# Optimization experiments

Hardware: AMD Instinct MI355X
Metric: run time of the kernel (lower is better)

## Reference

```python
import jax, jax.numpy as jnp
import numpy as np
from jax import lax

DEPTH = 3  # signature truncation depth
B, L, I, H, O = 256, 512, 32, 16, 10
SIG_DIM = H + H**2 + H**3  # 4368 = signatory.signature_channels(16, 3)


def setup_inputs() -> dict:
    key = jax.random.key(0)
    ks = jax.random.split(key, 7)
    s = 1.0 / np.sqrt(H).astype(np.float32)
    sf = 1.0 / np.sqrt(SIG_DIM).astype(np.float32)
    return {
        "X": jax.random.normal(ks[0], (B, L, I), jnp.float32),
        "W_ih": jax.random.uniform(ks[1], (4 * H, I), jnp.float32, -s, s),
        "W_hh": jax.random.uniform(ks[2], (4 * H, H), jnp.float32, -s, s),
        "b_ih": jax.random.uniform(ks[3], (4 * H,), jnp.float32, -s, s),
        "b_hh": jax.random.uniform(ks[4], (4 * H,), jnp.float32, -s, s),
        "fc_w": jax.random.uniform(ks[5], (O, SIG_DIM), jnp.float32, -sf, sf),
        "fc_b": jax.random.uniform(ks[6], (O,), jnp.float32, -sf, sf),
    }


def _lstm(X, W_ih, W_hh, b_ih, b_hh):
    # torch nn.LSTM, single layer, batch_first, gate order (i, f, g, o)
    b, l, _ = X.shape
    h0 = jnp.zeros((b, H), X.dtype)
    c0 = jnp.zeros((b, H), X.dtype)
    # precompute input projection for all timesteps: [L, B, 4H]
    xw = jnp.swapaxes(jnp.einsum('bli,gi->blg', X, W_ih) + b_ih + b_hh, 0, 1)

    def step(carry, xw_t):
        h, c = carry
        gates = xw_t + h @ W_hh.T
        i, f, g, o = jnp.split(gates, 4, axis=-1)
        c = jax.nn.sigmoid(f) * c + jax.nn.sigmoid(i) * jnp.tanh(g)
        h = jax.nn.sigmoid(o) * jnp.tanh(c)
        return (h, c), h

    _, hs = lax.scan(step, (h0, c0), xw)  # hs: [L, B, H]
    return jnp.swapaxes(hs, 0, 1)  # [B, L, H]


def _outer(a, b):
    # batched flattened tensor product: [B, m] x [B, n] -> [B, m*n]
    return (a[:, :, None] * b[:, None, :]).reshape(a.shape[0], -1)


def _signature(h, depth):
    # signatory.signature: Chen's identity scan over path increments,
    # returns concatenated levels 1..depth: [B, C + C^2 + ... + C^depth]
    b, l, c = h.shape
    dx = jnp.swapaxes(h[:, 1:] - h[:, :-1], 0, 1)  # [L-1, B, C]
    S0 = tuple(jnp.zeros((b, c ** (k + 1)), h.dtype) for k in range(depth))

    def step(S, d):
        # exp(d) levels: e_k = d^{tensor k} / k!
        e = [d]
        for k in range(2, depth + 1):
            e.append(_outer(e[-1], d) / k)
        # S <- S (x) exp(d), truncated:  newS_k = S_k + sum_{j=1..k-1} S_{k-j} (x) e_j + e_k
        newS = []
        for k in range(1, depth + 1):
            acc = S[k - 1] + e[k - 1]
            for j in range(1, k):
                acc = acc + _outer(S[k - j - 1], e[j - 1])
            newS.append(acc)
        return tuple(newS), None

    S, _ = lax.scan(step, S0, dx)
    return jnp.concatenate(S, axis=-1)  # [B, SIG_DIM]


def reference(X, W_ih, W_hh, b_ih, b_hh, fc_w, fc_b):
    hseq = _lstm(X, W_ih, W_hh, b_ih, b_hh)           # [B, L, H]
    sig = _signature(hseq, DEPTH)                      # [B, SIG_DIM]
    out = sig @ fc_w.T + fc_b                          # [B, O]
    return out.reshape(-1, O)
```

## Files before the change

### kernel.cpp

```cpp
#include <hip/hip_runtime.h>

#define NB 256
#define NL 512
#define NI 32
#define NH 16
#define NG 64
#define SIGD 4368

__device__ __forceinline__ float RL(float v, int lane) {
  return __builtin_bit_cast(float, __builtin_amdgcn_readlane(__builtin_bit_cast(int, v), lane));
}
template<int CTRL>
__device__ __forceinline__ float QB(float v) {
  return __builtin_bit_cast(float, __builtin_amdgcn_update_dpp(
      0, __builtin_bit_cast(int, v), CTRL, 0xF, 0xF, true));
}
__device__ __forceinline__ int cutf(int k) {
  switch (k) {
    case 1: return 71;  case 2: return 142; case 3: return 212; case 4: return 282;
    case 5: return 352; case 6: return 422; case 7: return 493; case 8: return 511;
    default: return 0;
  }
}

__global__ __launch_bounds__(512, 1) void k_main(const float* __restrict__ X,
    const float* __restrict__ Wih, const float* __restrict__ bih,
    const float* __restrict__ bhh, const float* __restrict__ Whh,
    const float* __restrict__ fcw, const float* __restrict__ fcb,
    float* __restrict__ out) {
  __shared__ __align__(16) float xwh[NL * NG];
  __shared__ __align__(16) float bnd[144];
  __shared__ int prog;
  int tid = threadIdx.x;
  int wv = tid >> 6;
  int ln = tid & 63;
  int b = blockIdx.x;

  if (tid == 0) prog = -1;

  {
    float w2[NI];
#pragma unroll
    for (int i = 0; i < 8; ++i) {
      float4 v = *(const float4*)(Wih + ln * NI + 4 * i);
      w2[4*i+0] = v.x; w2[4*i+1] = v.y; w2[4*i+2] = v.z; w2[4*i+3] = v.w;
    }
    float bias = bih[ln] + bhh[ln];
    const float* xb = X + (size_t)b * NL * NI;
#pragma unroll 4
    for (int t = 64 * wv; t < 64 * (wv + 1); ++t) {
      const float4* xr = (const float4*)(xb + t * NI);
      float x0 = bias, x1 = 0.f, x2 = 0.f, x3 = 0.f;
#pragma unroll
      for (int i = 0; i < 8; ++i) {
        float4 xv = xr[i];
        x0 += xv.x * w2[4*i+0]; x1 += xv.y * w2[4*i+1];
        x2 += xv.z * w2[4*i+2]; x3 += xv.w * w2[4*i+3];
      }
      xwh[t * NG + ln] = (x0 + x1) + (x2 + x3);
    }
  }
  __syncthreads();

  if (wv == 0) {
    const int q = ln & 3;
    const int j = ln >> 2;
    const int gmem = q * 16 + j;
    float w[NH];
#pragma unroll
    for (int qq = 0; qq < 4; ++qq) {
      float4 v = *(const float4*)(Whh + gmem * NH + 4 * qq);
      w[4*qq+0] = v.x; w[4*qq+1] = v.y; w[4*qq+2] = v.z; w[4*qq+3] = v.w;
    }
    const bool isg = (q == 2);
    const float K  = isg ? 2.885390082f : -1.442695041f;
    const float Av = isg ? -2.0f : 1.0f;
    const float Bv = isg ? 1.0f : 0.0f;
    float c = 0.0f, hval = 0.0f;
    float xpre[4];
#pragma unroll
    for (int k = 0; k < 4; ++k) xpre[k] = xwh[k * NG + gmem];
    for (int tb = 0; tb < NL; tb += 16) {
#pragma unroll
      for (int k = 0; k < 16; ++k) {
        int t = tb + k;
        float xval = xpre[k & 3];
        float a0 = xval, a1 = 0.f, a2 = 0.f, a3 = 0.f;
#pragma unroll
        for (int jj = 0; jj < 4; ++jj) {
          a0 += RL(hval, 16*jj + 0)  * w[4*jj + 0];
          a1 += RL(hval, 16*jj + 4)  * w[4*jj + 1];
          a2 += RL(hval, 16*jj + 8)  * w[4*jj + 2];
          a3 += RL(hval, 16*jj + 12) * w[4*jj + 3];
        }
        if (t + 4 < NL) xpre[k & 3] = xwh[(t + 4) * NG + gmem];
        float acc = (a0 + a1) + (a2 + a3);
        float e = __builtin_amdgcn_exp2f(K * acc);
        float r = __builtin_amdgcn_rcpf(1.0f + e);
        float val = __builtin_fmaf(Av, r, Bv);
        float iv = QB<0x00>(val);
        float fv = QB<0x55>(val);
        float gv = QB<0xAA>(val);
        float ov = QB<0xFF>(val);
        c = __builtin_fmaf(fv, c, iv * gv);
        float e2 = __builtin_amdgcn_exp2f(2.885390082f * c);
        float tc = __builtin_fmaf(-2.0f, __builtin_amdgcn_rcpf(1.0f + e2), 1.0f);
        hval = ov * tc;
        if (q == 0) xwh[t * NG + j] = hval;
      }
      __asm__ __volatile__("" ::: "memory");
      if (ln == 0) *(volatile int*)&prog = tb + 15;
    }
  }

  const int bi = ln & 15;
  const int hi = ln >> 4;
  const int ch = (wv == 0) ? 7 : (wv - 1);
  int ts = cutf(ch);
  int te = cutf(ch + 1);
  while (*(volatile int*)&prog < ts) __builtin_amdgcn_s_sleep(1);
  __asm__ __volatile__("" ::: "memory");

  float s3[4][16];
  float s2[4] = {0.f, 0.f, 0.f, 0.f};
#pragma unroll
  for (int m = 0; m < 4; ++m)
#pragma unroll
    for (int cc = 0; cc < 16; ++cc) s3[m][cc] = 0.f;
  float hc[16];
#pragma unroll
  for (int qq = 0; qq < 4; ++qq) {
    float4 v = *(const float4*)(xwh + ts * NG + 4 * qq);
    hc[4*qq+0]=v.x; hc[4*qq+1]=v.y; hc[4*qq+2]=v.z; hc[4*qq+3]=v.w;
  }
  float hcb = xwh[ts * NG + bi];
  float hca[4], h0a[4];
#pragma unroll
  for (int m = 0; m < 4; ++m) { hca[m] = xwh[ts * NG + 4 * m + hi]; h0a[m] = hca[m]; }
  for (int t = ts; t < te; ++t) {
    while (*(volatile int*)&prog < t + 1) __builtin_amdgcn_s_sleep(1);
    __asm__ __volatile__("" ::: "memory");
    const float* rn = xwh + (t + 1) * NG;
    float hn[16];
#pragma unroll
    for (int qq = 0; qq < 4; ++qq) {
      float4 v = *(const float4*)(rn + 4 * qq);
      hn[4*qq+0]=v.x; hn[4*qq+1]=v.y; hn[4*qq+2]=v.z; hn[4*qq+3]=v.w;
    }
    float hnb = rn[bi];
    float d[16];
#pragma unroll
    for (int cc = 0; cc < 16; ++cc) d[cc] = hn[cc] - hc[cc];
    float db = hnb - hcb;
    float P[4];
#pragma unroll
    for (int m = 0; m < 4; ++m) {
      float hna = rn[4 * m + hi];
      float da = hna - hca[m];
      float s1 = hca[m] - h0a[m];
      P[m] = s2[m] + db * (0.5f * s1 + 0.166666666667f * da);
      s2[m] += db * (s1 + 0.5f * da);
      hca[m] = hna;
    }
#pragma unroll
    for (int m = 0; m < 4; ++m)
#pragma unroll
      for (int cc = 0; cc < 16; ++cc)
        s3[m][cc] += P[m] * d[cc];
#pragma unroll
    for (int cc = 0; cc < 16; ++cc) hc[cc] = hn[cc];
    hcb = hnb;
  }
  __syncthreads();

  if (tid < 144) {
    int k = tid >> 4, j = tid & 15;
    bnd[tid] = xwh[cutf(k) * NG + j];
  }
  __syncthreads();

  float* slot0 = xwh;
  float* slot1 = xwh + 4352;
  float* sigb  = xwh + 8704;
  auto writeSlot = [&](float* slot) {
#pragma unroll
    for (int m = 0; m < 4; ++m) slot[64 * m + ln] = s2[m];
    float* s3s = slot + 256;
#pragma unroll
    for (int m = 0; m < 4; ++m)
#pragma unroll
      for (int cc = 0; cc < 16; ++cc)
        s3s[64 * ln + ((m * 16 + cc) ^ (ln & 31))] = s3[m][cc];
  };
  auto combineSlot = [&](const float* slot, int as_, int ae_, int bs_, int be_) {
    const float* s2b = slot;
    const float* s3b = slot + 256;
    float s1b[16];
#pragma unroll
    for (int cc = 0; cc < 16; ++cc) s1b[cc] = bnd[be_ * 16 + cc] - bnd[bs_ * 16 + cc];
    float s1bb = bnd[be_ * 16 + bi] - bnd[bs_ * 16 + bi];
    float s1aa[4];
#pragma unroll
    for (int m = 0; m < 4; ++m) {
      int a = 4 * m + hi;
      s1aa[m] = bnd[ae_ * 16 + a] - bnd[as_ * 16 + a];
    }
    float row[16];
#pragma unroll
    for (int cc = 0; cc < 16; ++cc) row[cc] = s2b[bi * 16 + cc];
#pragma unroll
    for (int m = 0; m < 4; ++m) {
      float s2bo = s2b[64 * m + ln];
#pragma unroll
      for (int cc = 0; cc < 16; ++cc)
        s3[m][cc] += s3b[64 * ln + ((m * 16 + cc) ^ (ln & 31))]
                   + s2[m] * s1b[cc] + s1aa[m] * row[cc];
      s2[m] += s2bo + s1aa[m] * s1bb;
    }
  };
  if (ch == 1) writeSlot(slot0);
  if (ch == 3) writeSlot(slot1);
  __syncthreads();
  if (ch == 0) combineSlot(slot0, 0, 1, 1, 2);
  if (ch == 2) combineSlot(slot1, 2, 3, 3, 4);
  __syncthreads();
  if (ch == 5) writeSlot(slot0);
  if (ch == 7) writeSlot(slot1);
  __syncthreads();
  if (ch == 4) combineSlot(slot0, 4, 5, 5, 6);
  if (ch == 6) combineSlot(slot1, 6, 7, 7, 8);
  __syncthreads();
  if (ch == 2) writeSlot(slot0);
  if (ch == 6) writeSlot(slot1);
  __syncthreads();
  if (ch == 0) combineSlot(slot0, 0, 2, 2, 4);
  if (ch == 4) combineSlot(slot1, 4, 6, 6, 8);
  __syncthreads();
  if (ch == 4) writeSlot(slot0);
  __syncthreads();
  if (ch == 0) {
    combineSlot(slot0, 0, 4, 4, 8);
    if (ln < 16) sigb[ln] = bnd[8 * 16 + ln] - bnd[ln];
#pragma unroll
    for (int m = 0; m < 4; ++m) sigb[16 + 64 * m + ln] = s2[m];
#pragma unroll
    for (int m = 0; m < 4; ++m) {
#pragma unroll
      for (int qq = 0; qq < 4; ++qq) {
        float4 v;
        v.x = s3[m][4*qq+0]; v.y = s3[m][4*qq+1]; v.z = s3[m][4*qq+2]; v.w = s3[m][4*qq+3];
        *(float4*)(sigb + 272 + 1024 * m + 256 * hi + 16 * bi + 4 * qq) = v;
      }
    }
  }
  __syncthreads();

  {
    float acc[10];
#pragma unroll
    for (int o = 0; o < 10; ++o) acc[o] = 0.f;
    for (int k = tid; k < SIGD; k += 512) {
      float s = sigb[k];
#pragma unroll
      for (int o = 0; o < 10; ++o) acc[o] += s * fcw[o * SIGD + k];
    }
#pragma unroll
    for (int o = 0; o < 10; ++o) {
      float v = acc[o];
#pragma unroll
      for (int off = 32; off > 0; off >>= 1) v += __shfl_down(v, off);
      if (ln == 0) bnd[wv * 10 + o] = v;
    }
    __syncthreads();
    if (tid < 10) {
      float s = fcb[tid];
#pragma unroll
      for (int w = 0; w < 8; ++w) s += bnd[w * 10 + tid];
      out[b * 10 + tid] = s;
    }
  }
}

extern "C" void kernel_launch(void* const* d_in, const int* in_sizes, int n_in,
                              void* d_out, int out_size, void* d_ws, size_t ws_size,
                              hipStream_t stream) {
  const float* X   = (const float*)d_in[0];
  const float* Wih = (const float*)d_in[1];
  const float* Whh = (const float*)d_in[2];
  const float* bih = (const float*)d_in[3];
  const float* bhh = (const float*)d_in[4];
  const float* fcw = (const float*)d_in[5];
  const float* fcb = (const float*)d_in[6];
  float* out = (float*)d_out;
  k_main<<<NB, 512, 0, stream>>>(X, Wih, bih, bhh, Whh, fcw, fcb, out);
}
```

Measured before the change: 208.0 us.

## Transpose LDS gate buffer to time-major and rebalance signature chunk schedule

```diff
diff --git a/kernel.cpp b/kernel.cpp
--- a/kernel.cpp
+++ b/kernel.cpp
@@ -6,6 +6,7 @@
 #define NH 16
 #define NG 64
 #define SIGD 4368
+#define XS 516
 
 __device__ __forceinline__ float RL(float v, int lane) {
   return __builtin_bit_cast(float, __builtin_amdgcn_readlane(__builtin_bit_cast(int, v), lane));
@@ -17,8 +18,8 @@
 }
 __device__ __forceinline__ int cutf(int k) {
   switch (k) {
-    case 1: return 71;  case 2: return 142; case 3: return 212; case 4: return 282;
-    case 5: return 352; case 6: return 422; case 7: return 493; case 8: return 511;
+    case 1: return 24;  case 2: return 102; case 3: return 180; case 4: return 258;
+    case 5: return 335; case 6: return 412; case 7: return 488; case 8: return 511;
     default: return 0;
   }
 }
@@ -28,7 +29,7 @@
     const float* __restrict__ bhh, const float* __restrict__ Whh,
     const float* __restrict__ fcw, const float* __restrict__ fcb,
     float* __restrict__ out) {
-  __shared__ __align__(16) float xwh[NL * NG];
+  __shared__ __align__(16) float xwT[NG * XS];
   __shared__ __align__(16) float bnd[144];
   __shared__ int prog;
   int tid = threadIdx.x;
@@ -57,7 +58,7 @@
         x0 += xv.x * w2[4*i+0]; x1 += xv.y * w2[4*i+1];
         x2 += xv.z * w2[4*i+2]; x3 += xv.w * w2[4*i+3];
       }
-      xwh[t * NG + ln] = (x0 + x1) + (x2 + x3);
+      xwT[ln * XS + t] = (x0 + x1) + (x2 + x3);
     }
   }
   __syncthreads();
@@ -76,16 +77,16 @@
     const float K  = isg ? 2.885390082f : -1.442695041f;
     const float Av = isg ? -2.0f : 1.0f;
     const float Bv = isg ? 1.0f : 0.0f;
+    const float* xt = xwT + gmem * XS;
+    float4 xq[4];
+#pragma unroll
+    for (int i = 0; i < 4; ++i) xq[i] = *(const float4*)(xt + 4 * i);
     float c = 0.0f, hval = 0.0f;
-    float xpre[4];
-#pragma unroll
-    for (int k = 0; k < 4; ++k) xpre[k] = xwh[k * NG + gmem];
     for (int tb = 0; tb < NL; tb += 16) {
 #pragma unroll
       for (int k = 0; k < 16; ++k) {
         int t = tb + k;
-        float xval = xpre[k & 3];
-        float a0 = xval, a1 = 0.f, a2 = 0.f, a3 = 0.f;
+        float a0 = 0.f, a1 = 0.f, a2 = 0.f, a3 = 0.f;
 #pragma unroll
         for (int jj = 0; jj < 4; ++jj) {
           a0 += RL(hval, 16*jj + 0)  * w[4*jj + 0];
@@ -93,8 +94,10 @@
           a2 += RL(hval, 16*jj + 8)  * w[4*jj + 2];
           a3 += RL(hval, 16*jj + 12) * w[4*jj + 3];
         }
-        if (t + 4 < NL) xpre[k & 3] = xwh[(t + 4) * NG + gmem];
-        float acc = (a0 + a1) + (a2 + a3);
+        float xval = ((const float*)xq)[k];
+        if ((k & 3) == 3 && t + 16 < NL)
+          xq[k >> 2] = *(const float4*)(xt + (t + 13));
+        float acc = ((a0 + a1) + (a2 + a3)) + xval;
         float e = __builtin_amdgcn_exp2f(K * acc);
         float r = __builtin_amdgcn_rcpf(1.0f + e);
         float val = __builtin_fmaf(Av, r, Bv);
@@ -106,7 +109,7 @@
         float e2 = __builtin_amdgcn_exp2f(2.885390082f * c);
         float tc = __builtin_fmaf(-2.0f, __builtin_amdgcn_rcpf(1.0f + e2), 1.0f);
         hval = ov * tc;
-        if (q == 0) xwh[t * NG + j] = hval;
+        xwT[j * XS + t] = hval;
       }
       __asm__ __volatile__("" ::: "memory");
       if (ln == 0) *(volatile int*)&prog = tb + 15;
@@ -115,10 +118,10 @@
 
   const int bi = ln & 15;
   const int hi = ln >> 4;
-  const int ch = (wv == 0) ? 7 : (wv - 1);
+  const int ch = wv;
   int ts = cutf(ch);
   int te = cutf(ch + 1);
-  while (*(volatile int*)&prog < ts) __builtin_amdgcn_s_sleep(1);
+  while (*(volatile int*)&prog < te) __builtin_amdgcn_s_sleep(2);
   __asm__ __volatile__("" ::: "memory");
 
   float s3[4][16];
@@ -129,25 +132,17 @@
     for (int cc = 0; cc < 16; ++cc) s3[m][cc] = 0.f;
   float hc[16];
 #pragma unroll
-  for (int qq = 0; qq < 4; ++qq) {
-    float4 v = *(const float4*)(xwh + ts * NG + 4 * qq);
-    hc[4*qq+0]=v.x; hc[4*qq+1]=v.y; hc[4*qq+2]=v.z; hc[4*qq+3]=v.w;
-  }
-  float hcb = xwh[ts * NG + bi];
+  for (int cc = 0; cc < 16; ++cc) hc[cc] = xwT[cc * XS + ts];
+  float hcb = xwT[bi * XS + ts];
   float hca[4], h0a[4];
 #pragma unroll
-  for (int m = 0; m < 4; ++m) { hca[m] = xwh[ts * NG + 4 * m + hi]; h0a[m] = hca[m]; }
+  for (int m = 0; m < 4; ++m) { hca[m] = xwT[(4 * m + hi) * XS + ts]; h0a[m] = hca[m]; }
   for (int t = ts; t < te; ++t) {
-    while (*(volatile int*)&prog < t + 1) __builtin_amdgcn_s_sleep(1);
-    __asm__ __volatile__("" ::: "memory");
-    const float* rn = xwh + (t + 1) * NG;
+    int tn = t + 1;
     float hn[16];
 #pragma unroll
-    for (int qq = 0; qq < 4; ++qq) {
-      float4 v = *(const float4*)(rn + 4 * qq);
-      hn[4*qq+0]=v.x; hn[4*qq+1]=v.y; hn[4*qq+2]=v.z; hn[4*qq+3]=v.w;
-    }
-    float hnb = rn[bi];
+    for (int cc = 0; cc < 16; ++cc) hn[cc] = xwT[cc * XS + tn];
+    float hnb = xwT[bi * XS + tn];
     float d[16];
 #pragma unroll
     for (int cc = 0; cc < 16; ++cc) d[cc] = hn[cc] - hc[cc];
@@ -155,7 +150,7 @@
     float P[4];
 #pragma unroll
     for (int m = 0; m < 4; ++m) {
-      float hna = rn[4 * m + hi];
+      float hna = xwT[(4 * m + hi) * XS + tn];
       float da = hna - hca[m];
       float s1 = hca[m] - h0a[m];
       P[m] = s2[m] + db * (0.5f * s1 + 0.166666666667f * da);
@@ -175,13 +170,13 @@
 
   if (tid < 144) {
     int k = tid >> 4, j = tid & 15;
-    bnd[tid] = xwh[cutf(k) * NG + j];
-  }
-  __syncthreads();
-
-  float* slot0 = xwh;
-  float* slot1 = xwh + 4352;
-  float* sigb  = xwh + 8704;
+    bnd[tid] = xwT[j * XS + cutf(k)];
+  }
+  __syncthreads();
+
+  float* slot0 = xwT;
+  float* slot1 = xwT + 4352;
+  float* sigb  = xwT + 8704;
   auto writeSlot = [&](float* slot) {
 #pragma unroll
     for (int m = 0; m < 4; ++m) slot[64 * m + ln] = s2[m];
```

Result: faster. 196.8 us (-5.4%).
